# Performance work log

Hardware: AMD Instinct MI355X
Metric: run time of the kernel (lower is better)

## Reference

```python
import jax, jax.numpy as jnp
import numpy as np

B, T, F, H = 512, 512, 32, 64  # batch, lag, n_features, hidden_sizes[0]


def _lstm_layer(x_seq, Wih, Whh, bih, bhh):
    """Single LSTM layer, batch_first input [B,T,Fin] -> [B,T,H].
    PyTorch gate order: i, f, g, o."""
    # Precompute input projections for all timesteps (one big GEMM)
    xg = jnp.einsum('btf,gf->btg', x_seq, Wih) + bih + bhh  # [B,T,4H]
    xg_t = jnp.transpose(xg, (1, 0, 2))  # [T,B,4H]
    h0 = jnp.zeros((x_seq.shape[0], Whh.shape[1]), x_seq.dtype)
    c0 = jnp.zeros_like(h0)

    def step(carry, g_t):
        h, c = carry
        gates = g_t + h @ Whh.T  # [B,4H]
        i, f, g, o = jnp.split(gates, 4, axis=-1)
        i = jax.nn.sigmoid(i)
        f = jax.nn.sigmoid(f)
        g = jnp.tanh(g)
        o = jax.nn.sigmoid(o)
        c = f * c + i * g
        h = o * jnp.tanh(c)
        return (h, c), h

    (_, _), hs = jax.lax.scan(step, (h0, c0), xg_t)  # hs: [T,B,H]
    return jnp.transpose(hs, (1, 0, 2))  # [B,T,H]


def setup_inputs() -> dict:
    key = jax.random.key(0)
    ks = jax.random.split(key, 12)
    s_in = 1.0 / np.sqrt(H)
    u = lambda k, shape: jax.random.uniform(k, shape, jnp.float32, -s_in, s_in)
    return {
        'x': jax.random.normal(ks[0], (B, T, F), jnp.float32),
        'Wih0': u(ks[1], (4 * H, F)),
        'Whh0': u(ks[2], (4 * H, H)),
        'bih0': u(ks[3], (4 * H,)),
        'bhh0': u(ks[4], (4 * H,)),
        'Wih1': u(ks[5], (4 * H, H)),
        'Whh1': u(ks[6], (4 * H, H)),
        'bih1': u(ks[7], (4 * H,)),
        'bhh1': u(ks[8], (4 * H,)),
        'fcW': u(ks[9], (1, H)),
        'fcb': u(ks[10], (1,)),
    }


def reference(x, Wih0, Whh0, bih0, bhh0, Wih1, Whh1, bih1, bhh1, fcW, fcb):
    h1 = _lstm_layer(x, Wih0, Whh0, bih0, bhh0)   # [B,T,H]
    h2 = _lstm_layer(h1, Wih1, Whh1, bih1, bhh1)  # [B,T,H]  (dropout=0 at inference)
    last = h2[:, -1, :]                           # [B,H]
    out = last @ fcW.T + fcb                      # [B,1]
    return out.squeeze(-1)                        # [B]
```

## Files before the change

kernel.cpp:

```cpp
#include <hip/hip_runtime.h>
#include <math.h>

#define Bsz 512
#define Tsz 512
#define Fin 32
#define Hd 64
#define CHUNK 32
#define NCH (Tsz / CHUNK)

typedef float v2f __attribute__((ext_vector_type(2)));

__device__ __forceinline__ float fsig(float x) {
    return 1.0f / (1.0f + __expf(-x));
}
__device__ __forceinline__ float ftanh(float x) {
    float ax = fabsf(x);
    float e  = __expf(-2.0f * ax);
    float t  = (1.0f - e) / (1.0f + e);
    return copysignf(t, x);
}

__global__ __launch_bounds__(256, 2)
void lstm_layer0(const float* __restrict__ x,
                 const float4* __restrict__ Wih4,
                 const float4* __restrict__ Whh4,
                 const float* __restrict__ bih,
                 const float* __restrict__ bhh,
                 float* __restrict__ h1out)
{
    __shared__ __align__(16) float xbuf[2][CHUNK * Fin];
    __shared__ __align__(16) float hbuf[CHUNK * Hd];
    __shared__ __align__(16) float hcopy[4][Hd];
    __shared__ float glds[2][Hd * 5];

    const int tid  = threadIdx.x;
    const int lane = tid & 63;
    const int wv   = tid >> 6;
    const int b    = blockIdx.x;

    float4 wih[8];
#pragma unroll
    for (int q = 0; q < 8; ++q) wih[q] = Wih4[tid * 8 + q];
    float4 whh[16];
#pragma unroll
    for (int q = 0; q < 16; ++q) whh[q] = Whh4[tid * 16 + q];
    const float bias = bih[tid] + bhh[tid];
    const bool is_tanh_gate = (wv == 2);

    float c = 0.0f;
    hcopy[wv][lane] = 0.0f;

    const float4* xsrc = (const float4*)(x + (size_t)b * Tsz * Fin);
    ((float4*)xbuf[0])[tid] = xsrc[tid];
    __syncthreads();

    for (int ci = 0; ci < NCH; ++ci) {
        const int cur = ci & 1;
        if (ci + 1 < NCH)
            ((float4*)xbuf[cur ^ 1])[tid] = xsrc[(ci + 1) * (CHUNK * Fin / 4) + tid];
#pragma unroll 1
        for (int ct = 0; ct < CHUNK; ++ct) {
            const int t = ci * CHUNK + ct;
            const int p = t & 1;
            const float4* xrow = (const float4*)&xbuf[cur][ct * Fin];
            const float4* hrow = (const float4*)&hcopy[wv][0];

            v2f acc0 = {bias, 0.0f};
            v2f acc1 = {0.0f, 0.0f};
#pragma unroll
            for (int q = 0; q < 8; ++q) {
                float4 xv = xrow[q];
                v2f b0 = {xv.x, xv.y}, b1 = {xv.z, xv.w};
                v2f w0 = {wih[q].x, wih[q].y}, w1 = {wih[q].z, wih[q].w};
                acc0 = __builtin_elementwise_fma(b0, w0, acc0);
                acc1 = __builtin_elementwise_fma(b1, w1, acc1);
            }
#pragma unroll
            for (int q = 0; q < 16; ++q) {
                float4 hv = hrow[q];
                v2f b0 = {hv.x, hv.y}, b1 = {hv.z, hv.w};
                v2f w0 = {whh[q].x, whh[q].y}, w1 = {whh[q].z, whh[q].w};
                acc0 = __builtin_elementwise_fma(b0, w0, acc0);
                acc1 = __builtin_elementwise_fma(b1, w1, acc1);
            }
            float a = (acc0.x + acc0.y) + (acc1.x + acc1.y);
            glds[p][lane * 5 + wv] = is_tanh_gate ? ftanh(a) : fsig(a);
            __syncthreads();
            float gi = glds[p][lane * 5 + 0];
            float gf = glds[p][lane * 5 + 1];
            float gg = glds[p][lane * 5 + 2];
            float go = glds[p][lane * 5 + 3];
            c = gf * c + gi * gg;
            float h = go * ftanh(c);
            hcopy[wv][lane] = h;
            if (wv == 0) hbuf[ct * Hd + lane] = h;
        }
        __syncthreads();
        float4* dst = (float4*)(h1out + (size_t)b * Tsz * Hd + (size_t)ci * CHUNK * Hd);
        dst[tid]       = ((const float4*)hbuf)[tid];
        dst[tid + 256] = ((const float4*)hbuf)[tid + 256];
    }
}

__global__ __launch_bounds__(256, 2)
void lstm_layer1_fc(const float* __restrict__ h1,
                    const float4* __restrict__ Wih4,
                    const float4* __restrict__ Whh4,
                    const float* __restrict__ bih,
                    const float* __restrict__ bhh,
                    const float* __restrict__ fcW,
                    const float* __restrict__ fcb,
                    float* __restrict__ out)
{
    __shared__ __align__(16) float xbuf[2][CHUNK * Hd];
    __shared__ __align__(16) float hcopy[4][Hd];
    __shared__ float glds[2][Hd * 5];

    const int tid  = threadIdx.x;
    const int lane = tid & 63;
    const int wv   = tid >> 6;
    const int b    = blockIdx.x;

    float4 wih[16];
#pragma unroll
    for (int q = 0; q < 16; ++q) wih[q] = Wih4[tid * 16 + q];
    float4 whh[16];
#pragma unroll
    for (int q = 0; q < 16; ++q) whh[q] = Whh4[tid * 16 + q];
    const float bias = bih[tid] + bhh[tid];
    const bool is_tanh_gate = (wv == 2);

    float c  = 0.0f;
    float hl = 0.0f;
    hcopy[wv][lane] = 0.0f;

    const float4* xsrc = (const float4*)(h1 + (size_t)b * Tsz * Hd);
    ((float4*)xbuf[0])[tid]       = xsrc[tid];
    ((float4*)xbuf[0])[tid + 256] = xsrc[tid + 256];
    __syncthreads();

    for (int ci = 0; ci < NCH; ++ci) {
        const int cur = ci & 1;
        if (ci + 1 < NCH) {
            ((float4*)xbuf[cur ^ 1])[tid]       = xsrc[(ci + 1) * (CHUNK * Hd / 4) + tid];
            ((float4*)xbuf[cur ^ 1])[tid + 256] = xsrc[(ci + 1) * (CHUNK * Hd / 4) + tid + 256];
        }
#pragma unroll 1
        for (int ct = 0; ct < CHUNK; ++ct) {
            const int t = ci * CHUNK + ct;
            const int p = t & 1;
            const float4* xrow = (const float4*)&xbuf[cur][ct * Hd];
            const float4* hrow = (const float4*)&hcopy[wv][0];

            v2f acc0 = {bias, 0.0f};
            v2f acc1 = {0.0f, 0.0f};
#pragma unroll
            for (int q = 0; q < 16; ++q) {
                float4 xv = xrow[q];
                v2f b0 = {xv.x, xv.y}, b1 = {xv.z, xv.w};
                v2f w0 = {wih[q].x, wih[q].y}, w1 = {wih[q].z, wih[q].w};
                acc0 = __builtin_elementwise_fma(b0, w0, acc0);
                acc1 = __builtin_elementwise_fma(b1, w1, acc1);
            }
#pragma unroll
            for (int q = 0; q < 16; ++q) {
                float4 hv = hrow[q];
                v2f b0 = {hv.x, hv.y}, b1 = {hv.z, hv.w};
                v2f w0 = {whh[q].x, whh[q].y}, w1 = {whh[q].z, whh[q].w};
                acc0 = __builtin_elementwise_fma(b0, w0, acc0);
                acc1 = __builtin_elementwise_fma(b1, w1, acc1);
            }
            float a = (acc0.x + acc0.y) + (acc1.x + acc1.y);
            glds[p][lane * 5 + wv] = is_tanh_gate ? ftanh(a) : fsig(a);
            __syncthreads();
            float gi = glds[p][lane * 5 + 0];
            float gf = glds[p][lane * 5 + 1];
            float gg = glds[p][lane * 5 + 2];
            float go = glds[p][lane * 5 + 3];
            c  = gf * c + gi * gg;
            hl = go * ftanh(c);
            hcopy[wv][lane] = hl;
        }
    }
    if (wv == 0) {
        float psum = hl * fcW[lane];
#pragma unroll
        for (int off = 32; off > 0; off >>= 1)
            psum += __shfl_down(psum, off);
        if (lane == 0) out[b] = psum + fcb[0];
    }
}

extern "C" void kernel_launch(void* const* d_in, const int* in_sizes, int n_in,
                              void* d_out, int out_size, void* d_ws, size_t ws_size,
                              hipStream_t stream)
{
    const float* x    = (const float*)d_in[0];
    const float* Wih0 = (const float*)d_in[1];
    const float* Whh0 = (const float*)d_in[2];
    const float* bih0 = (const float*)d_in[3];
    const float* bhh0 = (const float*)d_in[4];
    const float* Wih1 = (const float*)d_in[5];
    const float* Whh1 = (const float*)d_in[6];
    const float* bih1 = (const float*)d_in[7];
    const float* bhh1 = (const float*)d_in[8];
    const float* fcW  = (const float*)d_in[9];
    const float* fcb  = (const float*)d_in[10];
    float* out = (float*)d_out;
    float* h1  = (float*)d_ws;

    lstm_layer0<<<dim3(Bsz), dim3(256), 0, stream>>>(
        x, (const float4*)Wih0, (const float4*)Whh0, bih0, bhh0, h1);
    lstm_layer1_fc<<<dim3(Bsz), dim3(256), 0, stream>>>(
        h1, (const float4*)Wih1, (const float4*)Whh1, bih1, bhh1, fcW, fcb, out);
}
```

Before: 841.1 us.

## Split LSTM into producer input-projection wave and consumer recurrence wave

Each block now uses two waves: one computes the input projection for the next timestep into a shared ring buffer, while the other holds all four gates' recurrent weights per hidden unit and runs the recurrence, computing all gates per lane. This removes the cross-wave gate exchange, the chunked staging of inputs and hidden outputs, and halves the threads per block. The cost is four times more serial FMA work per lane on the critical path, very high register pressure, and lower occupancy.

New measurement: 1.021 ms. +21.4%, slower.

```diff
diff --git a/kernel.cpp b/kernel.cpp
--- a/kernel.cpp
+++ b/kernel.cpp
@@ -5,22 +5,17 @@
 #define Tsz 512
 #define Fin 32
 #define Hd 64
-#define CHUNK 32
-#define NCH (Tsz / CHUNK)
 
 typedef float v2f __attribute__((ext_vector_type(2)));
 
-__device__ __forceinline__ float fsig(float x) {
-    return 1.0f / (1.0f + __expf(-x));
-}
-__device__ __forceinline__ float ftanh(float x) {
-    float ax = fabsf(x);
-    float e  = __expf(-2.0f * ax);
-    float t  = (1.0f - e) / (1.0f + e);
-    return copysignf(t, x);
-}
-
-__global__ __launch_bounds__(256, 2)
+__device__ __forceinline__ float fsig(float x){ return 1.0f/(1.0f+__expf(-x)); }
+__device__ __forceinline__ float ftanh(float x){
+    float ax=fabsf(x); float e=__expf(-2.0f*ax);
+    float t=(1.0f-e)/(1.0f+e); return copysignf(t,x);
+}
+
+
+__global__ __launch_bounds__(128, 1)
 void lstm_layer0(const float* __restrict__ x,
                  const float4* __restrict__ Wih4,
                  const float4* __restrict__ Whh4,
@@ -28,81 +23,110 @@
                  const float* __restrict__ bhh,
                  float* __restrict__ h1out)
 {
-    __shared__ __align__(16) float xbuf[2][CHUNK * Fin];
-    __shared__ __align__(16) float hbuf[CHUNK * Hd];
-    __shared__ __align__(16) float hcopy[4][Hd];
-    __shared__ float glds[2][Hd * 5];
-
-    const int tid  = threadIdx.x;
-    const int lane = tid & 63;
-    const int wv   = tid >> 6;
-    const int b    = blockIdx.x;
-
-    float4 wih[8];
-#pragma unroll
-    for (int q = 0; q < 8; ++q) wih[q] = Wih4[tid * 8 + q];
-    float4 whh[16];
-#pragma unroll
-    for (int q = 0; q < 16; ++q) whh[q] = Whh4[tid * 16 + q];
-    const float bias = bih[tid] + bhh[tid];
-    const bool is_tanh_gate = (wv == 2);
-
-    float c = 0.0f;
-    hcopy[wv][lane] = 0.0f;
-
-    const float4* xsrc = (const float4*)(x + (size_t)b * Tsz * Fin);
-    ((float4*)xbuf[0])[tid] = xsrc[tid];
-    __syncthreads();
-
-    for (int ci = 0; ci < NCH; ++ci) {
-        const int cur = ci & 1;
-        if (ci + 1 < NCH)
-            ((float4*)xbuf[cur ^ 1])[tid] = xsrc[(ci + 1) * (CHUNK * Fin / 4) + tid];
-#pragma unroll 1
-        for (int ct = 0; ct < CHUNK; ++ct) {
-            const int t = ci * CHUNK + ct;
-            const int p = t & 1;
-            const float4* xrow = (const float4*)&xbuf[cur][ct * Fin];
-            const float4* hrow = (const float4*)&hcopy[wv][0];
-
-            v2f acc0 = {bias, 0.0f};
-            v2f acc1 = {0.0f, 0.0f};
-#pragma unroll
-            for (int q = 0; q < 8; ++q) {
-                float4 xv = xrow[q];
-                v2f b0 = {xv.x, xv.y}, b1 = {xv.z, xv.w};
-                v2f w0 = {wih[q].x, wih[q].y}, w1 = {wih[q].z, wih[q].w};
-                acc0 = __builtin_elementwise_fma(b0, w0, acc0);
-                acc1 = __builtin_elementwise_fma(b1, w1, acc1);
-            }
-#pragma unroll
-            for (int q = 0; q < 16; ++q) {
-                float4 hv = hrow[q];
-                v2f b0 = {hv.x, hv.y}, b1 = {hv.z, hv.w};
-                v2f w0 = {whh[q].x, whh[q].y}, w1 = {whh[q].z, whh[q].w};
-                acc0 = __builtin_elementwise_fma(b0, w0, acc0);
-                acc1 = __builtin_elementwise_fma(b1, w1, acc1);
-            }
-            float a = (acc0.x + acc0.y) + (acc1.x + acc1.y);
-            glds[p][lane * 5 + wv] = is_tanh_gate ? ftanh(a) : fsig(a);
-            __syncthreads();
-            float gi = glds[p][lane * 5 + 0];
-            float gf = glds[p][lane * 5 + 1];
-            float gg = glds[p][lane * 5 + 2];
-            float go = glds[p][lane * 5 + 3];
-            c = gf * c + gi * gg;
-            float h = go * ftanh(c);
-            hcopy[wv][lane] = h;
-            if (wv == 0) hbuf[ct * Hd + lane] = h;
+    __shared__ float4 pring[4][Hd];
+    __shared__ __align__(16) float harr[Hd];
+
+    const int tid=threadIdx.x, lane=tid&63, wv=tid>>6, b=blockIdx.x;
+
+    float4 wq[4][16];
+    float4 bq[16];
+    float4 nx[8];
+    float  b4[4];
+    float4 pr = {0.f,0.f,0.f,0.f};
+    float  c = 0.f, hl = 0.f;
+
+    const float4* xg = (const float4*)(x + (size_t)b*Tsz*Fin);
+    float* h1row = h1out + (size_t)b*Tsz*Hd;
+
+    if (wv==0){
+        #pragma unroll
+        for (int g=0; g<4; ++g){
+            const int row = g*Hd + lane;
+            #pragma unroll
+            for (int q=0; q<8; ++q) wq[g][q] = Wih4[row*(Fin/4)+q];
+            b4[g] = bih[row] + bhh[row];
+        }
+        #pragma unroll
+        for (int q=0; q<8; ++q) bq[q] = xg[q];
+    } else {
+        #pragma unroll
+        for (int g=0; g<4; ++g){
+            const int row = g*Hd + lane;
+            #pragma unroll
+            for (int q=0; q<16; ++q) wq[g][q] = Whh4[row*(Hd/4)+q];
+        }
+        #pragma unroll
+        for (int q=0; q<16; ++q) bq[q] = float4{0.f,0.f,0.f,0.f};
+    }
+
+    #pragma unroll 1
+    for (int s=0; s<Tsz+2; ++s){
+        if (wv==0){
+            if (s < Tsz){
+                if (s+1 < Tsz){
+                    #pragma unroll
+                    for (int q=0; q<8; ++q) nx[q] = xg[(s+1)*(Fin/4)+q];
+                }
+                v2f a0[4], a1[4];
+                #pragma unroll
+                for (int g=0; g<4; ++g){ a0[g] = v2f{b4[g], 0.f}; a1[g] = v2f{0.f,0.f}; }
+                #pragma unroll
+                for (int q=0; q<8; ++q){
+                    v2f u = {bq[q].x, bq[q].y};
+                    v2f v = {bq[q].z, bq[q].w};
+                    #pragma unroll
+                    for (int g=0; g<4; ++g){
+                        v2f w0 = {wq[g][q].x, wq[g][q].y};
+                        v2f w1 = {wq[g][q].z, wq[g][q].w};
+                        a0[g] = __builtin_elementwise_fma(u, w0, a0[g]);
+                        a1[g] = __builtin_elementwise_fma(v, w1, a1[g]);
+                    }
+                }
+                float4 p;
+                p.x = (a0[0].x+a0[0].y) + (a1[0].x+a1[0].y);
+                p.y = (a0[1].x+a0[1].y) + (a1[1].x+a1[1].y);
+                p.z = (a0[2].x+a0[2].y) + (a1[2].x+a1[2].y);
+                p.w = (a0[3].x+a0[3].y) + (a1[3].x+a1[3].y);
+                pring[s&3][lane] = p;
+                #pragma unroll
+                for (int q=0; q<8; ++q) bq[q] = nx[q];
+            }
+        } else {
+            if (s >= 2){
+                const int t = s-2;
+                v2f a0[4], a1[4];
+                #pragma unroll
+                for (int g=0; g<4; ++g){ a0[g]=v2f{0.f,0.f}; a1[g]=v2f{0.f,0.f}; }
+                #pragma unroll
+                for (int q=0; q<16; ++q){
+                    v2f u = {bq[q].x, bq[q].y};
+                    v2f v = {bq[q].z, bq[q].w};
+                    #pragma unroll
+                    for (int g=0; g<4; ++g){
+                        v2f w0 = {wq[g][q].x, wq[g][q].y};
+                        v2f w1 = {wq[g][q].z, wq[g][q].w};
+                        a0[g] = __builtin_elementwise_fma(u, w0, a0[g]);
+                        a1[g] = __builtin_elementwise_fma(v, w1, a1[g]);
+                    }
+                }
+                float gi = fsig (pr.x + (a0[0].x+a0[0].y) + (a1[0].x+a1[0].y));
+                float gf = fsig (pr.y + (a0[1].x+a0[1].y) + (a1[1].x+a1[1].y));
+                float gg = ftanh(pr.z + (a0[2].x+a0[2].y) + (a1[2].x+a1[2].y));
+                float go = fsig (pr.w + (a0[3].x+a0[3].y) + (a1[3].x+a1[3].y));
+                c  = gf*c + gi*gg;
+                hl = go*ftanh(c);
+                h1row[t*Hd + lane] = hl;
+                harr[lane] = hl;
+                #pragma unroll
+                for (int q=0; q<16; ++q) bq[q] = ((const float4*)harr)[q];
+            }
+            if (s>=1 && s<=Tsz) pr = pring[(s-1)&3][lane];
         }
         __syncthreads();
-        float4* dst = (float4*)(h1out + (size_t)b * Tsz * Hd + (size_t)ci * CHUNK * Hd);
-        dst[tid]       = ((const float4*)hbuf)[tid];
-        dst[tid + 256] = ((const float4*)hbuf)[tid + 256];
-    }
-}
-
-__global__ __launch_bounds__(256, 2)
+    }
+}
+
+__global__ __launch_bounds__(128, 1)
 void lstm_layer1_fc(const float* __restrict__ h1,
                     const float4* __restrict__ Wih4,
                     const float4* __restrict__ Whh4,
@@ -112,82 +136,110 @@
                     const float* __restrict__ fcb,
                     float* __restrict__ out)
 {
-    __shared__ __align__(16) float xbuf[2][CHUNK * Hd];
-    __shared__ __align__(16) float hcopy[4][Hd];
-    __shared__ float glds[2][Hd * 5];
-
-    const int tid  = threadIdx.x;
-    const int lane = tid & 63;
-    const int wv   = tid >> 6;
-    const int b    = blockIdx.x;
-
-    float4 wih[16];
-#pragma unroll
-    for (int q = 0; q < 16; ++q) wih[q] = Wih4[tid * 16 + q];
-    float4 whh[16];
-#pragma unroll
-    for (int q = 0; q < 16; ++q) whh[q] = Whh4[tid * 16 + q];
-    const float bias = bih[tid] + bhh[tid];
-    const bool is_tanh_gate = (wv == 2);
-
-    float c  = 0.0f;
-    float hl = 0.0f;
-    hcopy[wv][lane] = 0.0f;
-
-    const float4* xsrc = (const float4*)(h1 + (size_t)b * Tsz * Hd);
-    ((float4*)xbuf[0])[tid]       = xsrc[tid];
-    ((float4*)xbuf[0])[tid + 256] = xsrc[tid + 256];
-    __syncthreads();
-
-    for (int ci = 0; ci < NCH; ++ci) {
-        const int cur = ci & 1;
-        if (ci + 1 < NCH) {
-            ((float4*)xbuf[cur ^ 1])[tid]       = xsrc[(ci + 1) * (CHUNK * Hd / 4) + tid];
-            ((float4*)xbuf[cur ^ 1])[tid + 256] = xsrc[(ci + 1) * (CHUNK * Hd / 4) + tid + 256];
-        }
-#pragma unroll 1
-        for (int ct = 0; ct < CHUNK; ++ct) {
-            const int t = ci * CHUNK + ct;
-            const int p = t & 1;
-            const float4* xrow = (const float4*)&xbuf[cur][ct * Hd];
-            const float4* hrow = (const float4*)&hcopy[wv][0];
-
-            v2f acc0 = {bias, 0.0f};
-            v2f acc1 = {0.0f, 0.0f};
-#pragma unroll
-            for (int q = 0; q < 16; ++q) {
-                float4 xv = xrow[q];
-                v2f b0 = {xv.x, xv.y}, b1 = {xv.z, xv.w};
-                v2f w0 = {wih[q].x, wih[q].y}, w1 = {wih[q].z, wih[q].w};
-                acc0 = __builtin_elementwise_fma(b0, w0, acc0);
-                acc1 = __builtin_elementwise_fma(b1, w1, acc1);
-            }
-#pragma unroll
-            for (int q = 0; q < 16; ++q) {
-                float4 hv = hrow[q];
-                v2f b0 = {hv.x, hv.y}, b1 = {hv.z, hv.w};
-                v2f w0 = {whh[q].x, whh[q].y}, w1 = {whh[q].z, whh[q].w};
-                acc0 = __builtin_elementwise_fma(b0, w0, acc0);
-                acc1 = __builtin_elementwise_fma(b1, w1, acc1);
-            }
-            float a = (acc0.x + acc0.y) + (acc1.x + acc1.y);
-            glds[p][lane * 5 + wv] = is_tanh_gate ? ftanh(a) : fsig(a);
-            __syncthreads();
-            float gi = glds[p][lane * 5 + 0];
-            float gf = glds[p][lane * 5 + 1];
-            float gg = glds[p][lane * 5 + 2];
-            float go = glds[p][lane * 5 + 3];
-            c  = gf * c + gi * gg;
-            hl = go * ftanh(c);
-            hcopy[wv][lane] = hl;
-        }
-    }
-    if (wv == 0) {
-        float psum = hl * fcW[lane];
-#pragma unroll
-        for (int off = 32; off > 0; off >>= 1)
-            psum += __shfl_down(psum, off);
-        if (lane == 0) out[b] = psum + fcb[0];
+    __shared__ float4 pring[4][Hd];
+    __shared__ __align__(16) float harr[Hd];
+
+    const int tid=threadIdx.x, lane=tid&63, wv=tid>>6, b=blockIdx.x;
+
+    float4 wq[4][16];
+    float4 bq[16];
+    float4 nx[16];
+    float  b4[4];
+    float4 pr = {0.f,0.f,0.f,0.f};
+    float  c = 0.f, hl = 0.f;
+
+    const float4* xg = (const float4*)(h1 + (size_t)b*Tsz*Hd);
+
+    if (wv==0){
+        #pragma unroll
+        for (int g=0; g<4; ++g){
+            const int row = g*Hd + lane;
+            #pragma unroll
+            for (int q=0; q<16; ++q) wq[g][q] = Wih4[row*(Hd/4)+q];
+            b4[g] = bih[row] + bhh[row];
+        }
+        #pragma unroll
+        for (int q=0; q<16; ++q) bq[q] = xg[q];
+    } else {
+        #pragma unroll
+        for (int g=0; g<4; ++g){
+            const int row = g*Hd + lane;
+            #pragma unroll
+            for (int q=0; q<16; ++q) wq[g][q] = Whh4[row*(Hd/4)+q];
+        }
+        #pragma unroll
+        for (int q=0; q<16; ++q) bq[q] = float4{0.f,0.f,0.f,0.f};
+    }
+
+    #pragma unroll 1
+    for (int s=0; s<Tsz+2; ++s){
+        if (wv==0){
+            if (s < Tsz){
+                if (s+1 < Tsz){
+                    #pragma unroll
+                    for (int q=0; q<16; ++q) nx[q] = xg[(s+1)*(Hd/4)+q];
+                }
+                v2f a0[4], a1[4];
+                #pragma unroll
+                for (int g=0; g<4; ++g){ a0[g] = v2f{b4[g], 0.f}; a1[g] = v2f{0.f,0.f}; }
+                #pragma unroll
+                for (int q=0; q<16; ++q){
+                    v2f u = {bq[q].x, bq[q].y};
+                    v2f v = {bq[q].z, bq[q].w};
+                    #pragma unroll
+                    for (int g=0; g<4; ++g){
+                        v2f w0 = {wq[g][q].x, wq[g][q].y};
+                        v2f w1 = {wq[g][q].z, wq[g][q].w};
+                        a0[g] = __builtin_elementwise_fma(u, w0, a0[g]);
+                        a1[g] = __builtin_elementwise_fma(v, w1, a1[g]);
+                    }
+                }
+                float4 p;
+                p.x = (a0[0].x+a0[0].y) + (a1[0].x+a1[0].y);
+                p.y = (a0[1].x+a0[1].y) + (a1[1].x+a1[1].y);
+                p.z = (a0[2].x+a0[2].y) + (a1[2].x+a1[2].y);
+                p.w = (a0[3].x+a0[3].y) + (a1[3].x+a1[3].y);
+                pring[s&3][lane] = p;
+                #pragma unroll
+                for (int q=0; q<16; ++q) bq[q] = nx[q];
+            }
+        } else {
+            if (s >= 2){
+                v2f a0[4], a1[4];
+                #pragma unroll
+                for (int g=0; g<4; ++g){ a0[g]=v2f{0.f,0.f}; a1[g]=v2f{0.f,0.f}; }
+                #pragma unroll
+                for (int q=0; q<16; ++q){
+                    v2f u = {bq[q].x, bq[q].y};
+                    v2f v = {bq[q].z, bq[q].w};
+                    #pragma unroll
+                    for (int g=0; g<4; ++g){
+                        v2f w0 = {wq[g][q].x, wq[g][q].y};
+                        v2f w1 = {wq[g][q].z, wq[g][q].w};
+                        a0[g] = __builtin_elementwise_fma(u, w0, a0[g]);
+                        a1[g] = __builtin_elementwise_fma(v, w1, a1[g]);
+                    }
+                }
+                float gi = fsig (pr.x + (a0[0].x+a0[0].y) + (a1[0].x+a1[0].y));
+                float gf = fsig (pr.y + (a0[1].x+a0[1].y) + (a1[1].x+a1[1].y));
+                float gg = ftanh(pr.z + (a0[2].x+a0[2].y) + (a1[2].x+a1[2].y));
+                float go = fsig (pr.w + (a0[3].x+a0[3].y) + (a1[3].x+a1[3].y));
+                c  = gf*c + gi*gg;
+                hl = go*ftanh(c);
+                harr[lane] = hl;
+                #pragma unroll
+                for (int q=0; q<16; ++q) bq[q] = ((const float4*)harr)[q];
+            }
+            if (s>=1 && s<=Tsz) pr = pring[(s-1)&3][lane];
+        }
+        __syncthreads();
+    }
+
+    if (wv==1){
+        float p = hl * fcW[lane];
+        #pragma unroll
+        for (int off=32; off>0; off>>=1) p += __shfl_down(p, off);
+        if (lane==0) out[b] = p + fcb[0];
     }
 }
 
@@ -209,8 +261,8 @@
     float* out = (float*)d_out;
     float* h1  = (float*)d_ws;
 
-    lstm_layer0<<<dim3(Bsz), dim3(256), 0, stream>>>(
+    lstm_layer0<<<dim3(Bsz), dim3(128), 0, stream>>>(
         x, (const float4*)Wih0, (const float4*)Whh0, bih0, bhh0, h1);
-    lstm_layer1_fc<<<dim3(Bsz), dim3(256), 0, stream>>>(
+    lstm_layer1_fc<<<dim3(Bsz), dim3(128), 0, stream>>>(
         h1, (const float4*)Wih1, (const float4*)Whh1, bih1, bhh1, fcW, fcb, out);
 }
```

## Split LSTM into input-projection and recurrent waves with software-pipelined ring buffer

Applied to the files above, without the earlier changes.

Each block is now split by role. Two waves compute the input projections for future timesteps into a 4-deep LDS ring. The other two waves own the recurrence: each computes two gate rows, exchanges partial gate sums through LDS, and broadcasts h across lanes with readlane instead of reading h from LDS. This takes the input GEMM off the serial critical path and shortens the per-step dependency chain. The costs are duplicated activation work on the recurrent waves, heavy register use (hs[64] plus 32 float4 weights) that may cause spills at launch_bounds(256,2), and 64 readlanes per step.

Result: slower. 1.233 ms (+46.6%).

```diff
diff --git a/kernel.cpp b/kernel.cpp
--- a/kernel.cpp
+++ b/kernel.cpp
@@ -3,191 +3,143 @@
 
 #define Bsz 512
 #define Tsz 512
-#define Fin 32
 #define Hd 64
-#define CHUNK 32
-#define NCH (Tsz / CHUNK)
 
 typedef float v2f __attribute__((ext_vector_type(2)));
 
-__device__ __forceinline__ float fsig(float x) {
-    return 1.0f / (1.0f + __expf(-x));
+__device__ __forceinline__ float fsig(float x){ return 1.0f/(1.0f+__expf(-x)); }
+__device__ __forceinline__ float ftanh(float x){
+    float ax=fabsf(x); float e=__expf(-2.0f*ax);
+    float t=(1.0f-e)/(1.0f+e); return copysignf(t,x);
 }
-__device__ __forceinline__ float ftanh(float x) {
-    float ax = fabsf(x);
-    float e  = __expf(-2.0f * ax);
-    float t  = (1.0f - e) / (1.0f + e);
-    return copysignf(t, x);
+__device__ __forceinline__ float rlane(float v, int k){
+    return __int_as_float(__builtin_amdgcn_readlane(__float_as_int(v), k));
 }
 
+
+template<int FINQ, bool STORE_H, bool DO_FC>
 __global__ __launch_bounds__(256, 2)
-void lstm_layer0(const float* __restrict__ x,
-                 const float4* __restrict__ Wih4,
-                 const float4* __restrict__ Whh4,
-                 const float* __restrict__ bih,
-                 const float* __restrict__ bhh,
-                 float* __restrict__ h1out)
+void lstm_layer(const float* __restrict__ xin,
+                const float4* __restrict__ Wih4,
+                const float4* __restrict__ Whh4,
+                const float* __restrict__ bih,
+                const float* __restrict__ bhh,
+                float* __restrict__ hout,
+                const float* __restrict__ fcW,
+                const float* __restrict__ fcb,
+                float* __restrict__ out)
 {
-    __shared__ __align__(16) float xbuf[2][CHUNK * Fin];
-    __shared__ __align__(16) float hbuf[CHUNK * Hd];
-    __shared__ __align__(16) float hcopy[4][Hd];
-    __shared__ float glds[2][Hd * 5];
+    __shared__ float2 ring[4][128];
+    __shared__ float2 exch[2][128];
 
     const int tid  = threadIdx.x;
     const int lane = tid & 63;
     const int wv   = tid >> 6;
     const int b    = blockIdx.x;
 
-    float4 wih[8];
-#pragma unroll
-    for (int q = 0; q < 8; ++q) wih[q] = Wih4[tid * 8 + q];
-    float4 whh[16];
-#pragma unroll
-    for (int q = 0; q < 16; ++q) whh[q] = Whh4[tid * 16 + q];
-    const float bias = bih[tid] + bhh[tid];
-    const bool is_tanh_gate = (wv == 2);
+    if (wv < 2) {
+        const int u  = wv;
+        const int rA = u * 128 + lane;
+        const int rB = u * 128 + 64 + lane;
+        float4 wA[FINQ], wB[FINQ];
+        #pragma unroll
+        for (int q = 0; q < FINQ; ++q) wA[q] = Wih4[rA * FINQ + q];
+        #pragma unroll
+        for (int q = 0; q < FINQ; ++q) wB[q] = Wih4[rB * FINQ + q];
+        const float bA = bih[rA] + bhh[rA];
+        const float bB = bih[rB] + bhh[rB];
 
-    float c = 0.0f;
-    hcopy[wv][lane] = 0.0f;
+        const float4* xg = (const float4*)(xin + (size_t)b * Tsz * (FINQ * 4));
+        float4 cur[FINQ], nxt[FINQ];
+        #pragma unroll
+        for (int q = 0; q < FINQ; ++q) cur[q] = xg[q];
 
-    const float4* xsrc = (const float4*)(x + (size_t)b * Tsz * Fin);
-    ((float4*)xbuf[0])[tid] = xsrc[tid];
-    __syncthreads();
+        #pragma unroll 1
+        for (int s = 0; s < Tsz + 3; ++s) {
+            if (s < Tsz) {
+                if (s + 1 < Tsz) {
+                    #pragma unroll
+                    for (int q = 0; q < FINQ; ++q) nxt[q] = xg[(s + 1) * FINQ + q];
+                }
+                v2f aA0 = {bA, 0.f}, aA1 = {0.f, 0.f};
+                v2f aB0 = {bB, 0.f}, aB1 = {0.f, 0.f};
+                #pragma unroll
+                for (int q = 0; q < FINQ; ++q) {
+                    v2f xu = {cur[q].x, cur[q].y};
+                    v2f xv = {cur[q].z, cur[q].w};
+                    aA0 = __builtin_elementwise_fma(xu, v2f{wA[q].x, wA[q].y}, aA0);
+                    aA1 = __builtin_elementwise_fma(xv, v2f{wA[q].z, wA[q].w}, aA1);
+                    aB0 = __builtin_elementwise_fma(xu, v2f{wB[q].x, wB[q].y}, aB0);
+                    aB1 = __builtin_elementwise_fma(xv, v2f{wB[q].z, wB[q].w}, aB1);
+                }
+                float pA = (aA0.x + aA0.y) + (aA1.x + aA1.y);
+                float pB = (aB0.x + aB0.y) + (aB1.x + aB1.y);
+                ring[s & 3][u * 64 + lane] = float2{pA, pB};
+                #pragma unroll
+                for (int q = 0; q < FINQ; ++q) cur[q] = nxt[q];
+            }
+            __syncthreads();
+        }
+    } else {
+        const int u  = wv - 2;
+        const int rA = u * 128 + lane;
+        const int rB = u * 128 + 64 + lane;
+        float4 hA[16], hB[16];
+        #pragma unroll
+        for (int q = 0; q < 16; ++q) hA[q] = Whh4[rA * 16 + q];
+        #pragma unroll
+        for (int q = 0; q < 16; ++q) hB[q] = Whh4[rB * 16 + q];
 
-    for (int ci = 0; ci < NCH; ++ci) {
-        const int cur = ci & 1;
-        if (ci + 1 < NCH)
-            ((float4*)xbuf[cur ^ 1])[tid] = xsrc[(ci + 1) * (CHUNK * Fin / 4) + tid];
-#pragma unroll 1
-        for (int ct = 0; ct < CHUNK; ++ct) {
-            const int t = ci * CHUNK + ct;
-            const int p = t & 1;
-            const float4* xrow = (const float4*)&xbuf[cur][ct * Fin];
-            const float4* hrow = (const float4*)&hcopy[wv][0];
+        float hs[64];
+        #pragma unroll
+        for (int k = 0; k < 64; ++k) hs[k] = 0.0f;
 
-            v2f acc0 = {bias, 0.0f};
-            v2f acc1 = {0.0f, 0.0f};
-#pragma unroll
-            for (int q = 0; q < 8; ++q) {
-                float4 xv = xrow[q];
-                v2f b0 = {xv.x, xv.y}, b1 = {xv.z, xv.w};
-                v2f w0 = {wih[q].x, wih[q].y}, w1 = {wih[q].z, wih[q].w};
-                acc0 = __builtin_elementwise_fma(b0, w0, acc0);
-                acc1 = __builtin_elementwise_fma(b1, w1, acc1);
+        float c = 0.f, hl = 0.f;
+        float pMyA = 0.f, pMyB = 0.f;
+        float* hrow = STORE_H ? (hout + (size_t)b * Tsz * Hd) : nullptr;
+
+        #pragma unroll 1
+        for (int s = 0; s < Tsz + 3; ++s) {
+            const int th = s - 3;
+            const int tp = s - 2;
+            if (th >= 0) {
+                float2 other = exch[(s - 1) & 1][(1 - u) * 64 + lane];
+                float pi, pf, pg, po;
+                if (u == 0) { pi = pMyA; pf = pMyB; pg = other.x; po = other.y; }
+                else        { pg = pMyA; po = pMyB; pi = other.x; pf = other.y; }
+                float gi = fsig(pi), gf = fsig(pf), gg = ftanh(pg), go = fsig(po);
+                c  = gf * c + gi * gg;
+                hl = go * ftanh(c);
+                if (STORE_H && u == 0) hrow[th * Hd + lane] = hl;
+                #pragma unroll
+                for (int k = 0; k < 64; ++k) hs[k] = rlane(hl, k);
             }
-#pragma unroll
-            for (int q = 0; q < 16; ++q) {
-                float4 hv = hrow[q];
-                v2f b0 = {hv.x, hv.y}, b1 = {hv.z, hv.w};
-                v2f w0 = {whh[q].x, whh[q].y}, w1 = {whh[q].z, whh[q].w};
-                acc0 = __builtin_elementwise_fma(b0, w0, acc0);
-                acc1 = __builtin_elementwise_fma(b1, w1, acc1);
+            if (tp >= 0 && tp < Tsz) {
+                v2f aA0 = {0.f, 0.f}, aA1 = {0.f, 0.f};
+                v2f aB0 = {0.f, 0.f}, aB1 = {0.f, 0.f};
+                #pragma unroll
+                for (int q = 0; q < 16; ++q) {
+                    v2f h0 = {hs[4 * q + 0], hs[4 * q + 1]};
+                    v2f h1 = {hs[4 * q + 2], hs[4 * q + 3]};
+                    aA0 = __builtin_elementwise_fma(h0, v2f{hA[q].x, hA[q].y}, aA0);
+                    aA1 = __builtin_elementwise_fma(h1, v2f{hA[q].z, hA[q].w}, aA1);
+                    aB0 = __builtin_elementwise_fma(h0, v2f{hB[q].x, hB[q].y}, aB0);
+                    aB1 = __builtin_elementwise_fma(h1, v2f{hB[q].z, hB[q].w}, aB1);
+                }
+                float2 rg = ring[tp & 3][u * 64 + lane];
+                pMyA = rg.x + (aA0.x + aA0.y) + (aA1.x + aA1.y);
+                pMyB = rg.y + (aB0.x + aB0.y) + (aB1.x + aB1.y);
+                exch[s & 1][u * 64 + lane] = float2{pMyA, pMyB};
             }
-            float a = (acc0.x + acc0.y) + (acc1.x + acc1.y);
-            glds[p][lane * 5 + wv] = is_tanh_gate ? ftanh(a) : fsig(a);
             __syncthreads();
-            float gi = glds[p][lane * 5 + 0];
-            float gf = glds[p][lane * 5 + 1];
-            float gg = glds[p][lane * 5 + 2];
-            float go = glds[p][lane * 5 + 3];
-            c = gf * c + gi * gg;
-            float h = go * ftanh(c);
-            hcopy[wv][lane] = h;
-            if (wv == 0) hbuf[ct * Hd + lane] = h;
         }
-        __syncthreads();
-        float4* dst = (float4*)(h1out + (size_t)b * Tsz * Hd + (size_t)ci * CHUNK * Hd);
-        dst[tid]       = ((const float4*)hbuf)[tid];
-        dst[tid + 256] = ((const float4*)hbuf)[tid + 256];
-    }
-}
 
-__global__ __launch_bounds__(256, 2)
-void lstm_layer1_fc(const float* __restrict__ h1,
-                    const float4* __restrict__ Wih4,
-                    const float4* __restrict__ Whh4,
-                    const float* __restrict__ bih,
-                    const float* __restrict__ bhh,
-                    const float* __restrict__ fcW,
-                    const float* __restrict__ fcb,
-                    float* __restrict__ out)
-{
-    __shared__ __align__(16) float xbuf[2][CHUNK * Hd];
-    __shared__ __align__(16) float hcopy[4][Hd];
-    __shared__ float glds[2][Hd * 5];
-
-    const int tid  = threadIdx.x;
-    const int lane = tid & 63;
-    const int wv   = tid >> 6;
-    const int b    = blockIdx.x;
-
-    float4 wih[16];
-#pragma unroll
-    for (int q = 0; q < 16; ++q) wih[q] = Wih4[tid * 16 + q];
-    float4 whh[16];
-#pragma unroll
-    for (int q = 0; q < 16; ++q) whh[q] = Whh4[tid * 16 + q];
-    const float bias = bih[tid] + bhh[tid];
-    const bool is_tanh_gate = (wv == 2);
-
-    float c  = 0.0f;
-    float hl = 0.0f;
-    hcopy[wv][lane] = 0.0f;
-
-    const float4* xsrc = (const float4*)(h1 + (size_t)b * Tsz * Hd);
-    ((float4*)xbuf[0])[tid]       = xsrc[tid];
-    ((float4*)xbuf[0])[tid + 256] = xsrc[tid + 256];
-    __syncthreads();
-
-    for (int ci = 0; ci < NCH; ++ci) {
-        const int cur = ci & 1;
-        if (ci + 1 < NCH) {
-            ((float4*)xbuf[cur ^ 1])[tid]       = xsrc[(ci + 1) * (CHUNK * Hd / 4) + tid];
-            ((float4*)xbuf[cur ^ 1])[tid + 256] = xsrc[(ci + 1) * (CHUNK * Hd / 4) + tid + 256];
+        if (DO_FC && u == 0) {
+            float p = hl * fcW[lane];
+            #pragma unroll
+            for (int off = 32; off > 0; off >>= 1) p += __shfl_down(p, off);
+            if (lane == 0) out[b] = p + fcb[0];
         }
-#pragma unroll 1
-        for (int ct = 0; ct < CHUNK; ++ct) {
-            const int t = ci * CHUNK + ct;
-            const int p = t & 1;
-            const float4* xrow = (const float4*)&xbuf[cur][ct * Hd];
-            const float4* hrow = (const float4*)&hcopy[wv][0];
-
-            v2f acc0 = {bias, 0.0f};
-            v2f acc1 = {0.0f, 0.0f};
-#pragma unroll
-            for (int q = 0; q < 16; ++q) {
-                float4 xv = xrow[q];
-                v2f b0 = {xv.x, xv.y}, b1 = {xv.z, xv.w};
-                v2f w0 = {wih[q].x, wih[q].y}, w1 = {wih[q].z, wih[q].w};
-                acc0 = __builtin_elementwise_fma(b0, w0, acc0);
-                acc1 = __builtin_elementwise_fma(b1, w1, acc1);
-            }
-#pragma unroll
-            for (int q = 0; q < 16; ++q) {
-                float4 hv = hrow[q];
-                v2f b0 = {hv.x, hv.y}, b1 = {hv.z, hv.w};
-                v2f w0 = {whh[q].x, whh[q].y}, w1 = {whh[q].z, whh[q].w};
-                acc0 = __builtin_elementwise_fma(b0, w0, acc0);
-                acc1 = __builtin_elementwise_fma(b1, w1, acc1);
-            }
-            float a = (acc0.x + acc0.y) + (acc1.x + acc1.y);
-            glds[p][lane * 5 + wv] = is_tanh_gate ? ftanh(a) : fsig(a);
-            __syncthreads();
-            float gi = glds[p][lane * 5 + 0];
-            float gf = glds[p][lane * 5 + 1];
-            float gg = glds[p][lane * 5 + 2];
-            float go = glds[p][lane * 5 + 3];
-            c  = gf * c + gi * gg;
-            hl = go * ftanh(c);
-            hcopy[wv][lane] = hl;
-        }
-    }
-    if (wv == 0) {
-        float psum = hl * fcW[lane];
-#pragma unroll
-        for (int off = 32; off > 0; off >>= 1)
-            psum += __shfl_down(psum, off);
-        if (lane == 0) out[b] = psum + fcb[0];
     }
 }
 
@@ -209,8 +161,10 @@
     float* out = (float*)d_out;
     float* h1  = (float*)d_ws;
 
-    lstm_layer0<<<dim3(Bsz), dim3(256), 0, stream>>>(
-        x, (const float4*)Wih0, (const float4*)Whh0, bih0, bhh0, h1);
-    lstm_layer1_fc<<<dim3(Bsz), dim3(256), 0, stream>>>(
-        h1, (const float4*)Wih1, (const float4*)Whh1, bih1, bhh1, fcW, fcb, out);
+    lstm_layer<8, true, false><<<dim3(Bsz), dim3(256), 0, stream>>>(
+        x, (const float4*)Wih0, (const float4*)Whh0, bih0, bhh0, h1,
+        nullptr, nullptr, nullptr);
+    lstm_layer<16, false, true><<<dim3(Bsz), dim3(256), 0, stream>>>(
+        h1, (const float4*)Wih1, (const float4*)Whh1, bih1, bhh1, nullptr,
+        fcW, fcb, out);
 }
```
